# Optimization experiments

Hardware: AMD Instinct MI355X
Metric: run time of the kernel (lower is better)

## Reference

```python
import jax, jax.numpy as jnp
import numpy as np

DIM = 1024
HEADS = 16
DIM_HEADS = DIM // HEADS  # 64
DIM_HIDDEN = DIM_HEADS * HEADS


def setup_inputs() -> dict:
    key = jax.random.key(0)
    k1, k2, k3, k4, k5 = jax.random.split(key, 5)
    b, t = 2, 2048
    x = jax.random.normal(k1, (b, t, DIM), dtype=jnp.float32)
    # torch nn.Linear weights are [out_features, in_features]
    s = DIM ** -0.5
    W_q = jax.random.normal(k2, (DIM_HIDDEN, DIM), dtype=jnp.float32) * s
    W_kv = jax.random.normal(k3, (2 * DIM_HIDDEN, DIM), dtype=jnp.float32) * s
    W_out = jax.random.normal(k4, (DIM, DIM_HIDDEN), dtype=jnp.float32) * s
    b_out = jax.random.normal(k5, (DIM,), dtype=jnp.float32) * 0.01
    return {"x": x, "W_q": W_q, "W_kv": W_kv, "W_out": W_out, "b_out": b_out}


def reference(x, W_q, W_kv, W_out, b_out):
    b, t, d = x.shape
    h, e = HEADS, DIM_HEADS
    # projections (Linear: x @ W.T)
    q = jnp.einsum('btd,fd->btf', x, W_q)
    kv = jnp.einsum('btd,fd->btf', x, W_kv)
    k, v = jnp.split(kv, 2, axis=-1)
    # split heads -> (b, h, t, e)
    split = lambda z: z.reshape(b, t, h, e).transpose(0, 2, 1, 3)
    q, k, v = split(q), split(k), split(v)
    # scaled dot-product attention; original uses exp/sum/div softmax
    scores = jnp.einsum('bhqe,bhke->bhqk', q, k) * (e ** -0.5)
    attn = jax.nn.softmax(scores, axis=-1)
    out = jnp.einsum('bhqk,bhke->bhqe', attn, v)
    out = out.transpose(0, 2, 1, 3).reshape(b, t, h * e)
    return jnp.einsum('btf,df->btd', out, W_out) + b_out
```

## Files before the change

### kernel.cpp

```cpp
#include <hip/hip_runtime.h>
#include <hip/hip_bf16.h>

#define BB   2
#define TT   2048
#define DD   1024
#define HH   16
#define EE   64
#define BT   4096

typedef __attribute__((ext_vector_type(8))) short bf16x8;
typedef __attribute__((ext_vector_type(4))) float floatx4;
typedef __attribute__((ext_vector_type(16))) float floatx16;

__device__ __forceinline__ unsigned short f2bf(float f) {
  unsigned int x = __float_as_uint(f);
  x += 0x7fffu + ((x >> 16) & 1u);
  return (unsigned short)(x >> 16);
}
__device__ __forceinline__ unsigned int pack2u(float a, float b) {
  union { __hip_bfloat162 h; unsigned int u; } r;
  r.h = __float22bfloat162_rn(make_float2(a, b));
  return r.u;
}
__device__ __forceinline__ uint4 pack8(const float4& a, const float4& b) {
  union { uint4 u; __hip_bfloat162 h[4]; } r;
  r.h[0] = __float22bfloat162_rn(make_float2(a.x, a.y));
  r.h[1] = __float22bfloat162_rn(make_float2(a.z, a.w));
  r.h[2] = __float22bfloat162_rn(make_float2(b.x, b.y));
  r.h[3] = __float22bfloat162_rn(make_float2(b.z, b.w));
  return r.u;
}
__device__ __forceinline__ void ld16(unsigned short* lds, const unsigned short* g) {
  __builtin_amdgcn_global_load_lds(
      (const __attribute__((address_space(1))) unsigned int*)g,
      (__attribute__((address_space(3))) unsigned int*)lds, 16, 0, 0);
}

#define GX   524288
#define GWQ  131072
#define GWKV 262144
#define GWO  131072

__global__ __launch_bounds__(256) void convert_kernel(
    const float* __restrict__ X,  const float* __restrict__ Wq,
    const float* __restrict__ Wkv, const float* __restrict__ Wout,
    unsigned short* __restrict__ Xb, unsigned short* __restrict__ Wb,
    unsigned short* __restrict__ Wob) {
  int g = blockIdx.x * 256 + threadIdx.x;
  const float* src; unsigned short* dst; int gi;
  if (g < GX)                        { src = X;    dst = Xb;  gi = g; }
  else if ((g -= GX) < GWQ)          { src = Wq;   dst = Wb;  gi = g; }
  else if ((g -= GWQ) < GWKV)        { src = Wkv;  dst = Wb + (size_t)GWQ * 8; gi = g; }
  else                               { src = Wout; dst = Wob; gi = g - GWKV; }
  const float4* s4 = reinterpret_cast<const float4*>(src) + (size_t)gi * 2;
  float4 a = s4[0], b = s4[1];
  reinterpret_cast<uint4*>(dst)[gi] = pack8(a, b);
}

__global__ __launch_bounds__(256) void gemm_qkv_mfma(
    const unsigned short* __restrict__ Xb,
    const unsigned short* __restrict__ Wb,
    unsigned short* __restrict__ Qh,
    unsigned short* __restrict__ Kh,
    unsigned short* __restrict__ Vt) {
  __shared__ __align__(16) unsigned short As[128 * 64];
  __shared__ __align__(16) unsigned short Bs[128 * 64];
  const int tid  = threadIdx.x;
  const int lane = tid & 63, w = tid >> 6;
  const int wm = w >> 1, wn = w & 1;
  const int q = lane >> 4, c = lane & 15;
  const int bm0 = blockIdx.y * 128;
  const int bn0 = blockIdx.x * 128;
  const unsigned short* Ag = Xb + (size_t)bm0 * DD;
  const unsigned short* Bg = Wb + (size_t)bn0 * DD;

  floatx4 acc[4][4];
#pragma unroll
  for (int i = 0; i < 4; ++i)
#pragma unroll
    for (int j = 0; j < 4; ++j) acc[i][j] = (floatx4){0.f, 0.f, 0.f, 0.f};

  int prow[4], pch[4];
#pragma unroll
  for (int t = 0; t < 4; ++t) {
    int s = (w * 4 + t) * 64 + lane;
    prow[t] = s >> 3;
    pch[t]  = (s & 7) ^ (prow[t] & 7);
  }
  int aoff[4][2], boff[4][2];
#pragma unroll
  for (int i = 0; i < 4; ++i)
#pragma unroll
    for (int h = 0; h < 2; ++h) {
      aoff[i][h] = (wm * 64 + i * 16 + c) * 64 + (((q + h * 4) ^ (c & 7)) << 3);
      boff[i][h] = (wn * 64 + i * 16 + c) * 64 + (((q + h * 4) ^ (c & 7)) << 3);
    }

  for (int kk = 0; kk < DD; kk += 64) {
    __syncthreads();
#pragma unroll
    for (int t = 0; t < 4; ++t) {
      int i = w * 4 + t;
      ld16(&As[i * 512], &Ag[(size_t)prow[t] * DD + kk + pch[t] * 8]);
      ld16(&Bs[i * 512], &Bg[(size_t)prow[t] * DD + kk + pch[t] * 8]);
    }
    __syncthreads();
    bf16x8 af[4][2], bfr[4][2];
#pragma unroll
    for (int i = 0; i < 4; ++i)
#pragma unroll
      for (int h = 0; h < 2; ++h) {
        af[i][h]  = *reinterpret_cast<const bf16x8*>(&As[aoff[i][h]]);
        bfr[i][h] = *reinterpret_cast<const bf16x8*>(&Bs[boff[i][h]]);
      }
#pragma unroll
    for (int i = 0; i < 4; ++i)
#pragma unroll
      for (int j = 0; j < 4; ++j) {
        acc[i][j] = __builtin_amdgcn_mfma_f32_16x16x32_bf16(af[i][0], bfr[j][0], acc[i][j], 0, 0, 0);
        acc[i][j] = __builtin_amdgcn_mfma_f32_16x16x32_bf16(af[i][1], bfr[j][1], acc[i][j], 0, 0, 0);
      }
  }

  const int region = bn0 >> 10;
  const float scl = (region == 0) ? 0.125f : 1.0f;
#pragma unroll
  for (int i = 0; i < 4; ++i) {
#pragma unroll
    for (int j = 0; j < 4; ++j) {
#pragma unroll
      for (int reg = 0; reg < 4; ++reg) {
        int m = bm0 + wm * 64 + i * 16 + q * 4 + reg;
        int n = bn0 + wn * 64 + j * 16 + c;
        int nb = n & 1023;
        int h = nb >> 6, e = nb & 63;
        int b = m >> 11, t = m & 2047;
        unsigned short v = f2bf(acc[i][j][reg] * scl);
        if (region == 0)      Qh[((size_t)((b * HH + h) * TT + t)) * EE + e] = v;
        else if (region == 1) Kh[((size_t)((b * HH + h) * TT + t)) * EE + e] = v;
        else                  Vt[((size_t)(b * HH + h)) * EE * TT + (size_t)e * TT + t] = v;
      }
    }
  }
}

#define LPP 72

__global__ __launch_bounds__(256) void attn_kernel(
    const unsigned short* __restrict__ Qh,
    const unsigned short* __restrict__ Kh,
    const unsigned short* __restrict__ Vtg,
    unsigned short* __restrict__ Aw) {
  __shared__ __align__(16) unsigned short Ks[64 * 64];
  __shared__ __align__(16) unsigned short Vs[64 * 64];
  __shared__ __align__(16) unsigned short Ps[128 * LPP];

  const int tid  = threadIdx.x;
  const int lane = tid & 63;
  const int w    = tid >> 6;
  const int n31  = lane & 31;
  const int g    = lane >> 5;

  const int qt = blockIdx.x;
  const int bh = blockIdx.y;
  const size_t base = (size_t)bh * TT * EE;
  const unsigned short* Qp = Qh + base + (size_t)qt * 128 * EE;
  const unsigned short* Kp = Kh + base;
  const unsigned short* Vp = Vtg + base;

  bf16x8 qf[4];
#pragma unroll
  for (int kc = 0; kc < 4; ++kc)
    qf[kc] = *reinterpret_cast<const bf16x8*>(
        &Qp[(size_t)(w * 32 + n31) * EE + kc * 16 + g * 8]);

  int srow[2], sch[2];
#pragma unroll
  for (int t = 0; t < 2; ++t) {
    int s = (w * 2 + t) * 64 + lane;
    srow[t] = s >> 3;
    sch[t]  = (s & 7) ^ (srow[t] & 7);
  }

  float l_sum = 0.0f;
  floatx16 o_acc[2];
  o_acc[0] = (floatx16)(0.0f);
  o_acc[1] = (floatx16)(0.0f);

  const int prow_w = (w * 32 + n31) * LPP;

  for (int kt = 0; kt < TT / 64; ++kt) {
    __syncthreads();
#pragma unroll
    for (int t = 0; t < 2; ++t) {
      int i = w * 2 + t;
      ld16(&Ks[i * 512], &Kp[(size_t)(kt * 64 + srow[t]) * EE + sch[t] * 8]);
      ld16(&Vs[i * 512], &Vp[(size_t)srow[t] * TT + kt * 64 + sch[t] * 8]);
    }
    __syncthreads();

    floatx16 sacc[2];
#pragma unroll
    for (int nt = 0; nt < 2; ++nt) {
      sacc[nt] = (floatx16)(0.0f);
      int krow = nt * 32 + n31;
#pragma unroll
      for (int kc = 0; kc < 4; ++kc) {
        int swch = (kc * 2 + g) ^ (krow & 7);
        bf16x8 kf = *reinterpret_cast<const bf16x8*>(&Ks[krow * 64 + swch * 8]);
        sacc[nt] = __builtin_amdgcn_mfma_f32_32x32x16_bf16(kf, qf[kc], sacc[nt], 0, 0, 0);
      }
    }

#pragma unroll
    for (int nt = 0; nt < 2; ++nt) {
#pragma unroll
      for (int r = 0; r < 4; ++r) {
        float p0 = __expf(sacc[nt][r * 4 + 0]);
        float p1 = __expf(sacc[nt][r * 4 + 1]);
        float p2 = __expf(sacc[nt][r * 4 + 2]);
        float p3 = __expf(sacc[nt][r * 4 + 3]);
        l_sum += (p0 + p1) + (p2 + p3);
        uint2 pk;
        pk.x = pack2u(p0, p1);
        pk.y = pack2u(p2, p3);
        *reinterpret_cast<uint2*>(&Ps[prow_w + nt * 32 + r * 8 + g * 4]) = pk;
      }
    }
    asm volatile("s_waitcnt lgkmcnt(0)" ::: "memory");

#pragma unroll
    for (int kc = 0; kc < 4; ++kc) {
      bf16x8 pf = *reinterpret_cast<const bf16x8*>(&Ps[prow_w + kc * 16 + g * 8]);
#pragma unroll
      for (int eh = 0; eh < 2; ++eh) {
        int vrow = eh * 32 + n31;
        int swch = (kc * 2 + g) ^ (vrow & 7);
        bf16x8 vf = *reinterpret_cast<const bf16x8*>(&Vs[vrow * 64 + swch * 8]);
        o_acc[eh] = __builtin_amdgcn_mfma_f32_32x32x16_bf16(pf, vf, o_acc[eh], 0, 0, 0);
      }
    }
  }

  l_sum += __shfl_xor(l_sum, 32, 64);

  const int b = bh >> 4, h = bh & 15;
#pragma unroll
  for (int eh = 0; eh < 2; ++eh) {
    int e = eh * 32 + n31;
#pragma unroll
    for (int reg = 0; reg < 16; ++reg) {
      int qrl = (reg & 3) + 8 * (reg >> 2) + 4 * g;
      float linv = 1.0f / __shfl(l_sum, qrl, 64);
      int t = qt * 128 + w * 32 + qrl;
      Aw[((size_t)(b * TT + t)) * DD + h * EE + e] = f2bf(o_acc[eh][reg] * linv);
    }
  }
}

__global__ __launch_bounds__(256) void gemm_out_mfma(
    const unsigned short* __restrict__ A,
    const unsigned short* __restrict__ Wob,
    const float* __restrict__ bias,
    float* __restrict__ out) {
  __shared__ __align__(16) unsigned short As[128 * 64];
  __shared__ __align__(16) unsigned short Bs[64 * 64];
  const int tid  = threadIdx.x;
  const int lane = tid & 63, w = tid >> 6;
  const int wm = w >> 1, wn = w & 1;
  const int q = lane >> 4, c = lane & 15;
  const int bm0 = blockIdx.y * 128;
  const int bn0 = blockIdx.x * 64;
  const unsigned short* Ag = A + (size_t)bm0 * DD;
  const unsigned short* Bg = Wob + (size_t)bn0 * DD;

  floatx4 acc[4][2];
#pragma unroll
  for (int i = 0; i < 4; ++i)
#pragma unroll
    for (int j = 0; j < 2; ++j) acc[i][j] = (floatx4){0.f, 0.f, 0.f, 0.f};

  int parow[4], pach[4];
#pragma unroll
  for (int t = 0; t < 4; ++t) {
    int s = (w * 4 + t) * 64 + lane;
    parow[t] = s >> 3;
    pach[t]  = (s & 7) ^ (parow[t] & 7);
  }
  int pbrow[2], pbch[2];
#pragma unroll
  for (int t = 0; t < 2; ++t) {
    int s = (w * 2 + t) * 64 + lane;
    pbrow[t] = s >> 3;
    pbch[t]  = (s & 7) ^ (pbrow[t] & 7);
  }

  for (int kk = 0; kk < DD; kk += 64) {
    __syncthreads();
#pragma unroll
    for (int t = 0; t < 4; ++t)
      ld16(&As[(w * 4 + t) * 512], &Ag[(size_t)parow[t] * DD + kk + pach[t] * 8]);
#pragma unroll
    for (int t = 0; t < 2; ++t)
      ld16(&Bs[(w * 2 + t) * 512], &Bg[(size_t)pbrow[t] * DD + kk + pbch[t] * 8]);
    __syncthreads();
    bf16x8 af[4][2], bfr[2][2];
#pragma unroll
    for (int h = 0; h < 2; ++h) {
      int ksw = ((q + h * 4) ^ (c & 7)) << 3;
#pragma unroll
      for (int i = 0; i < 4; ++i)
        af[i][h] = *reinterpret_cast<const bf16x8*>(&As[(wm * 64 + i * 16 + c) * 64 + ksw]);
#pragma unroll
      for (int j = 0; j < 2; ++j)
        bfr[j][h] = *reinterpret_cast<const bf16x8*>(&Bs[(wn * 32 + j * 16 + c) * 64 + ksw]);
    }
#pragma unroll
    for (int i = 0; i < 4; ++i)
#pragma unroll
      for (int j = 0; j < 2; ++j) {
        acc[i][j] = __builtin_amdgcn_mfma_f32_16x16x32_bf16(af[i][0], bfr[j][0], acc[i][j], 0, 0, 0);
        acc[i][j] = __builtin_amdgcn_mfma_f32_16x16x32_bf16(af[i][1], bfr[j][1], acc[i][j], 0, 0, 0);
      }
  }

#pragma unroll
  for (int i = 0; i < 4; ++i) {
#pragma unroll
    for (int j = 0; j < 2; ++j) {
      int n = bn0 + wn * 32 + j * 16 + c;
      float bv = bias[n];
#pragma unroll
      for (int reg = 0; reg < 4; ++reg) {
        int m = bm0 + wm * 64 + i * 16 + q * 4 + reg;
        out[(size_t)m * DD + n] = acc[i][j][reg] + bv;
      }
    }
  }
}

extern "C" void kernel_launch(void* const* d_in, const int* in_sizes, int n_in,
                              void* d_out, int out_size, void* d_ws, size_t ws_size,
                              hipStream_t stream) {
  const float* X    = (const float*)d_in[0];
  const float* Wq   = (const float*)d_in[1];
  const float* Wkv  = (const float*)d_in[2];
  const float* Wout = (const float*)d_in[3];
  const float* bout = (const float*)d_in[4];
  float* out = (float*)d_out;

  unsigned short* Qh  = (unsigned short*)d_ws;
  unsigned short* Kh  = Qh + (size_t)BT * DD;
  unsigned short* Vt  = Kh + (size_t)BT * DD;
  unsigned short* Aw  = Vt + (size_t)BT * DD;
  unsigned short* Xb  = Aw;
  unsigned short* Wb  = Aw + (size_t)BT * DD;
  unsigned short* Wob = Wb + (size_t)3 * 1024 * DD;

  convert_kernel<<<dim3(4096), 256, 0, stream>>>(X, Wq, Wkv, Wout, Xb, Wb, Wob);
  gemm_qkv_mfma<<<dim3(24, 32), 256, 0, stream>>>(Xb, Wb, Qh, Kh, Vt);
  attn_kernel<<<dim3(16, 32), 256, 0, stream>>>(Qh, Kh, Vt, Aw);
  gemm_out_mfma<<<dim3(16, 32), 256, 0, stream>>>(Aw, Wob, bout, out);
}
```

Before: 200.8 us.

## Double-buffer K/V tiles and keep P in registers in attention kernel

The attention kernel drops to 128 threads, with each wave handling 64 query rows as two 32-row slices. K/V tiles are double-buffered in shared memory, and the next tile is prefetched with a vmcnt wait before the barrier. The softmax numerators are packed straight into MFMA A-operand registers instead of being staged through an LDS P buffer, with V fragments gathered to match. This is meant to hide global load latency and cut LDS traffic and barriers, at the cost of fewer waves per block, higher register pressure and possible occupancy loss.

Result: slower. 205.0 us (+2.1%).

```diff
diff --git a/kernel.cpp b/kernel.cpp
--- a/kernel.cpp
+++ b/kernel.cpp
@@ -144,16 +144,13 @@
   }
 }
 
-#define LPP 72
-
-__global__ __launch_bounds__(256) void attn_kernel(
+__global__ __launch_bounds__(128) void attn_kernel(
     const unsigned short* __restrict__ Qh,
     const unsigned short* __restrict__ Kh,
     const unsigned short* __restrict__ Vtg,
     unsigned short* __restrict__ Aw) {
-  __shared__ __align__(16) unsigned short Ks[64 * 64];
-  __shared__ __align__(16) unsigned short Vs[64 * 64];
-  __shared__ __align__(16) unsigned short Ps[128 * LPP];
+  __shared__ __align__(16) unsigned short Ks[2][64 * 64];
+  __shared__ __align__(16) unsigned short Vs[2][64 * 64];
 
   const int tid  = threadIdx.x;
   const int lane = tid & 63;
@@ -164,96 +161,120 @@
   const int qt = blockIdx.x;
   const int bh = blockIdx.y;
   const size_t base = (size_t)bh * TT * EE;
-  const unsigned short* Qp = Qh + base + (size_t)qt * 128 * EE;
+  const unsigned short* Qp = Qh + base + (size_t)(qt * 128 + w * 64) * EE;
   const unsigned short* Kp = Kh + base;
   const unsigned short* Vp = Vtg + base;
 
-  bf16x8 qf[4];
-#pragma unroll
-  for (int kc = 0; kc < 4; ++kc)
-    qf[kc] = *reinterpret_cast<const bf16x8*>(
-        &Qp[(size_t)(w * 32 + n31) * EE + kc * 16 + g * 8]);
-
-  int srow[2], sch[2];
-#pragma unroll
-  for (int t = 0; t < 2; ++t) {
-    int s = (w * 2 + t) * 64 + lane;
+  bf16x8 qf[2][4];
+#pragma unroll
+  for (int s = 0; s < 2; ++s)
+#pragma unroll
+    for (int kc = 0; kc < 4; ++kc)
+      qf[s][kc] = *reinterpret_cast<const bf16x8*>(
+          &Qp[(size_t)(s * 32 + n31) * EE + kc * 16 + g * 8]);
+
+  int srow[4], sch[4];
+#pragma unroll
+  for (int t = 0; t < 4; ++t) {
+    int s = (t * 2 + w) * 64 + lane;
     srow[t] = s >> 3;
     sch[t]  = (s & 7) ^ (srow[t] & 7);
   }
 
-  float l_sum = 0.0f;
-  floatx16 o_acc[2];
-  o_acc[0] = (floatx16)(0.0f);
-  o_acc[1] = (floatx16)(0.0f);
-
-  const int prow_w = (w * 32 + n31) * LPP;
-
-  for (int kt = 0; kt < TT / 64; ++kt) {
-    __syncthreads();
-#pragma unroll
-    for (int t = 0; t < 2; ++t) {
-      int i = w * 2 + t;
-      ld16(&Ks[i * 512], &Kp[(size_t)(kt * 64 + srow[t]) * EE + sch[t] * 8]);
-      ld16(&Vs[i * 512], &Vp[(size_t)srow[t] * TT + kt * 64 + sch[t] * 8]);
-    }
-    __syncthreads();
-
-    floatx16 sacc[2];
-#pragma unroll
-    for (int nt = 0; nt < 2; ++nt) {
-      sacc[nt] = (floatx16)(0.0f);
-      int krow = nt * 32 + n31;
-#pragma unroll
-      for (int kc = 0; kc < 4; ++kc) {
-        int swch = (kc * 2 + g) ^ (krow & 7);
-        bf16x8 kf = *reinterpret_cast<const bf16x8*>(&Ks[krow * 64 + swch * 8]);
-        sacc[nt] = __builtin_amdgcn_mfma_f32_32x32x16_bf16(kf, qf[kc], sacc[nt], 0, 0, 0);
-      }
-    }
-
-#pragma unroll
-    for (int nt = 0; nt < 2; ++nt) {
-#pragma unroll
-      for (int r = 0; r < 4; ++r) {
-        float p0 = __expf(sacc[nt][r * 4 + 0]);
-        float p1 = __expf(sacc[nt][r * 4 + 1]);
-        float p2 = __expf(sacc[nt][r * 4 + 2]);
-        float p3 = __expf(sacc[nt][r * 4 + 3]);
-        l_sum += (p0 + p1) + (p2 + p3);
-        uint2 pk;
-        pk.x = pack2u(p0, p1);
-        pk.y = pack2u(p2, p3);
-        *reinterpret_cast<uint2*>(&Ps[prow_w + nt * 32 + r * 8 + g * 4]) = pk;
-      }
-    }
-    asm volatile("s_waitcnt lgkmcnt(0)" ::: "memory");
-
-#pragma unroll
-    for (int kc = 0; kc < 4; ++kc) {
-      bf16x8 pf = *reinterpret_cast<const bf16x8*>(&Ps[prow_w + kc * 16 + g * 8]);
-#pragma unroll
-      for (int eh = 0; eh < 2; ++eh) {
-        int vrow = eh * 32 + n31;
-        int swch = (kc * 2 + g) ^ (vrow & 7);
-        bf16x8 vf = *reinterpret_cast<const bf16x8*>(&Vs[vrow * 64 + swch * 8]);
-        o_acc[eh] = __builtin_amdgcn_mfma_f32_32x32x16_bf16(pf, vf, o_acc[eh], 0, 0, 0);
-      }
-    }
-  }
-
-  l_sum += __shfl_xor(l_sum, 32, 64);
+  floatx16 o_acc[2][2];
+  o_acc[0][0] = (floatx16)(0.0f); o_acc[0][1] = (floatx16)(0.0f);
+  o_acc[1][0] = (floatx16)(0.0f); o_acc[1][1] = (floatx16)(0.0f);
+  float l_sum[2] = {0.0f, 0.0f};
+
+#pragma unroll
+  for (int t = 0; t < 4; ++t) {
+    ld16(&Ks[0][(t * 2 + w) * 512], &Kp[(size_t)srow[t] * EE + sch[t] * 8]);
+    ld16(&Vs[0][(t * 2 + w) * 512], &Vp[(size_t)srow[t] * TT + sch[t] * 8]);
+  }
+
+  for (int kt = 0; kt < 32; ++kt) {
+    const int p  = kt & 1;
+    const int nk = (kt + 1) & 31;
+#pragma unroll
+    for (int t = 0; t < 4; ++t) {
+      ld16(&Ks[p ^ 1][(t * 2 + w) * 512], &Kp[(size_t)(nk * 64 + srow[t]) * EE + sch[t] * 8]);
+      ld16(&Vs[p ^ 1][(t * 2 + w) * 512], &Vp[(size_t)srow[t] * TT + nk * 64 + sch[t] * 8]);
+    }
+    asm volatile("s_waitcnt vmcnt(8)" ::: "memory");
+    asm volatile("s_barrier" ::: "memory");
+
+    const unsigned short* Kb = Ks[p];
+    const unsigned short* Vb = Vs[p];
+
+#pragma unroll
+    for (int s = 0; s < 2; ++s) {
+      floatx16 sacc[2];
+      sacc[0] = (floatx16)(0.0f);
+      sacc[1] = (floatx16)(0.0f);
+#pragma unroll
+      for (int nt = 0; nt < 2; ++nt) {
+        const int krow = nt * 32 + n31;
+#pragma unroll
+        for (int kc = 0; kc < 4; ++kc) {
+          const int swch = (kc * 2 + g) ^ (krow & 7);
+          bf16x8 kf = *reinterpret_cast<const bf16x8*>(&Kb[krow * 64 + swch * 8]);
+          sacc[nt] = __builtin_amdgcn_mfma_f32_32x32x16_bf16(kf, qf[s][kc], sacc[nt], 0, 0, 0);
+        }
+      }
+      unsigned int pp[2][8] __attribute__((aligned(16)));
+#pragma unroll
+      for (int nt = 0; nt < 2; ++nt)
+#pragma unroll
+        for (int r = 0; r < 8; ++r) {
+          float e0 = __expf(sacc[nt][2 * r]);
+          float e1 = __expf(sacc[nt][2 * r + 1]);
+          l_sum[s] += e0 + e1;
+          pp[nt][r] = pack2u(e0, e1);
+        }
+#pragma unroll
+      for (int nt = 0; nt < 2; ++nt)
+#pragma unroll
+        for (int kcp = 0; kcp < 2; ++kcp) {
+          union { unsigned int u[4]; bf16x8 v; } pf;
+          pf.u[0] = pp[nt][4 * kcp + 0]; pf.u[1] = pp[nt][4 * kcp + 1];
+          pf.u[2] = pp[nt][4 * kcp + 2]; pf.u[3] = pp[nt][4 * kcp + 3];
+#pragma unroll
+          for (int eh = 0; eh < 2; ++eh) {
+            const int vrow = eh * 32 + n31;
+            const int c0 = (nt * 4 + 2 * kcp)     ^ (vrow & 7);
+            const int c1 = (nt * 4 + 2 * kcp + 1) ^ (vrow & 7);
+            uint2 v0 = *reinterpret_cast<const uint2*>(&Vb[vrow * 64 + c0 * 8 + g * 4]);
+            uint2 v1 = *reinterpret_cast<const uint2*>(&Vb[vrow * 64 + c1 * 8 + g * 4]);
+            union { unsigned int u[4]; bf16x8 v; } vf;
+            vf.u[0] = v0.x; vf.u[1] = v0.y; vf.u[2] = v1.x; vf.u[3] = v1.y;
+            o_acc[s][eh] = __builtin_amdgcn_mfma_f32_32x32x16_bf16(pf.v, vf.v, o_acc[s][eh], 0, 0, 0);
+          }
+        }
+    }
+    asm volatile("s_barrier" ::: "memory");
+  }
+
+  l_sum[0] += __shfl_xor(l_sum[0], 32, 64);
+  l_sum[1] += __shfl_xor(l_sum[1], 32, 64);
 
   const int b = bh >> 4, h = bh & 15;
 #pragma unroll
-  for (int eh = 0; eh < 2; ++eh) {
-    int e = eh * 32 + n31;
+  for (int s = 0; s < 2; ++s) {
+    float linv[16];
 #pragma unroll
     for (int reg = 0; reg < 16; ++reg) {
       int qrl = (reg & 3) + 8 * (reg >> 2) + 4 * g;
-      float linv = 1.0f / __shfl(l_sum, qrl, 64);
-      int t = qt * 128 + w * 32 + qrl;
-      Aw[((size_t)(b * TT + t)) * DD + h * EE + e] = f2bf(o_acc[eh][reg] * linv);
+      linv[reg] = 1.0f / __shfl(l_sum[s], qrl, 64);
+    }
+#pragma unroll
+    for (int eh = 0; eh < 2; ++eh) {
+      int e = eh * 32 + n31;
+#pragma unroll
+      for (int reg = 0; reg < 16; ++reg) {
+        int qrl = (reg & 3) + 8 * (reg >> 2) + 4 * g;
+        int t = qt * 128 + w * 64 + s * 32 + qrl;
+        Aw[((size_t)(b * TT + t)) * DD + h * EE + e] = f2bf(o_acc[s][eh][reg] * linv[reg]);
+      }
     }
   }
 }
@@ -359,6 +380,6 @@
 
   convert_kernel<<<dim3(4096), 256, 0, stream>>>(X, Wq, Wkv, Wout, Xb, Wb, Wob);
   gemm_qkv_mfma<<<dim3(24, 32), 256, 0, stream>>>(Xb, Wb, Qh, Kh, Vt);
-  attn_kernel<<<dim3(16, 32), 256, 0, stream>>>(Qh, Kh, Vt, Aw);
+  attn_kernel<<<dim3(16, 32), 128, 0, stream>>>(Qh, Kh, Vt, Aw);
   gemm_out_mfma<<<dim3(16, 32), 256, 0, stream>>>(Aw, Wob, bout, out);
 }
```
